# Kernel tuning notes

Measured on AMD Instinct MI355X. Metric: run time of the kernel, lower is better.

Reference implementation:

```python
import jax, jax.numpy as jnp
import numpy as np

ALPHA = 0.5    # SpikeAct surrogate width (act_fun(alpha=0.5))
DECAY = 0.2    # membrane decay
THRESH = 0.5   # firing threshold (requires_grad=False -> constant)


@jax.custom_vjp
def spike_act(x):
    # Heaviside spike with rectangular surrogate gradient
    return (x > 0).astype(x.dtype)

def _sa_fwd(x):
    return spike_act(x), x

def _sa_bwd(x, g):
    return (g * (jnp.abs(x) < ALPHA).astype(g.dtype),)

spike_act.defvjp(_sa_fwd, _sa_bwd)


@jax.custom_vjp
def ei_act(x):
    # EI sign gate with straight-through gradient
    return jnp.sign(x)

def _ei_fwd(x):
    return ei_act(x), None

def _ei_bwd(_, g):
    return (g,)

ei_act.defvjp(_ei_fwd, _ei_bwd)


def conv2d(x, w, b):
    # x: [B,C,H,W], w: [O,I,kh,kw] (OIHW), SAME padding, stride 1
    y = jax.lax.conv_general_dilated(
        x, w, window_strides=(1, 1), padding='SAME',
        dimension_numbers=('NCHW', 'OIHW', 'NCHW'))
    return y + b[None, :, None, None]


def setup_inputs() -> dict:
    key = jax.random.key(0)
    k0, k1, k2 = jax.random.split(key, 3)
    T, B, C, H, W, K = 8, 16, 128, 32, 32, 5
    fan_in = C * K * K
    x = jax.random.normal(k0, (T, B, C, H, W), jnp.float32)
    back_w = jax.random.normal(k1, (C, C, K, K), jnp.float32) / np.float32(np.sqrt(fan_in))
    back_b = jnp.zeros((C,), jnp.float32)
    ei_w = jax.random.normal(k2, (C, C, K, K), jnp.float32) / np.float32(np.sqrt(fan_in))
    ei_b = jnp.zeros((C,), jnp.float32)
    return {"x": x, "back_w": back_w, "back_b": back_b, "ei_w": ei_w, "ei_b": ei_b}


def reference(x, back_w, back_b, ei_w, ei_b):
    # x: [T,B,C,H,W] -> spikes over time [T,B,C,H,W]
    state_shape = x.shape[1:]
    mem0 = jnp.zeros(state_shape, x.dtype)
    spike0 = jnp.zeros(state_shape, x.dtype)

    def step(carry, xt):
        mem, spike = carry
        # integral: decayed mem + feedback-conv sigmoid gate * input
        mem = DECAY * mem + jax.nn.sigmoid(conv2d(spike, back_w, back_b)) * xt
        # calc_spike (if_ei=True path)
        ei_gate = ei_act(conv2d(mem, ei_w, ei_b))
        s = spike_act(mem - THRESH)
        mem = mem * (1.0 - s)
        spike = ei_gate * s
        return (mem, spike), spike

    _, spikes = jax.lax.scan(step, (mem0, spike0), x)
    return spikes
```

## Files before the change

### kernel.cpp

```cpp
#include <hip/hip_runtime.h>
#include <math.h>

#define TDIM 512
#define CCH  128
#define HW   32
#define OCT  4
#define NPH  32
#define PSW  36
#define PPL  1296
#define NCHK 11
#define LDSPH 2816


__device__ __forceinline__ void gll16(const float* g, float* l) {
    __builtin_amdgcn_global_load_lds(
        (const __attribute__((address_space(1))) unsigned int*)g,
        (__attribute__((address_space(3))) unsigned int*)l, 16, 0, 0);
}

template<int EPI>
__global__ __launch_bounds__(TDIM, 2) void lif_conv(
    const float* __restrict__ cpad,
    const float* __restrict__ wgt,
    const float* __restrict__ bias,
    const float* __restrict__ xin,
    float* __restrict__ pad0,
    float* __restrict__ outn,
    float* __restrict__ pad1,
    int first)
{
    const int ocg  = blockIdx.x;
    const int b    = blockIdx.y;
    const int oc0  = ocg * OCT;
    const int tid  = threadIdx.x;
    const int team = tid >> 8;
    const int lt   = tid & 255;
    const int rl   = lt >> 3;
    const int cl   = (lt & 7) * 4;
    const int wv   = (tid >> 6) & 3;
    const int lane = tid & 63;

    const int steam = __builtin_amdgcn_readfirstlane(team);

    __shared__ __align__(16) float s_in[2 * 2 * LDSPH];

    float acc[OCT][4];
#pragma unroll
    for (int oc = 0; oc < OCT; ++oc)
#pragma unroll
        for (int j = 0; j < 4; ++j) acc[oc][j] = 0.f;

    if (!(EPI == 0 && first)) {
        const int icb  = team * 64;
        const int sicb = steam * 64;
        float* lbase = s_in + steam * (2 * LDSPH);

        {
            const float* ps = cpad + ((size_t)b * CCH + icb) * PPL;
            for (int j = wv; j < NCHK; j += 4)
                gll16(ps + j * 256 + lane * 4, lbase + j * 256);
        }

        for (int ph = 0; ph < NPH; ++ph) {
            __syncthreads();
            if (ph < NPH - 1) {
                const float* ps = cpad + ((size_t)b * CCH + icb + (ph + 1) * 2) * PPL;
                float* ld = lbase + ((ph + 1) & 1) * LDSPH;
                for (int j = wv; j < NCHK; j += 4)
                    gll16(ps + j * 256 + lane * 4, ld + j * 256);
            }
            const float* tin = lbase + (ph & 1) * LDSPH;
#pragma unroll
            for (int ici = 0; ici < 2; ++ici) {
                float win5[5][8];
#pragma unroll
                for (int kh = 0; kh < 5; ++kh) {
                    const float* src = tin + ici * PPL + (rl + kh) * PSW + cl;
                    float4 a  = *(const float4*)src;
                    float4 c2 = *(const float4*)(src + 4);
                    win5[kh][0] = a.x;  win5[kh][1] = a.y;  win5[kh][2] = a.z;  win5[kh][3] = a.w;
                    win5[kh][4] = c2.x; win5[kh][5] = c2.y; win5[kh][6] = c2.z; win5[kh][7] = c2.w;
                }
                const float* wb = wgt + ((size_t)oc0 * CCH + sicb + ph * 2 + ici) * 25;
#pragma unroll
                for (int oc = 0; oc < OCT; ++oc) {
                    const float* wo = wb + oc * (CCH * 25);
#pragma unroll
                    for (int kh = 0; kh < 5; ++kh) {
#pragma unroll
                        for (int kw = 0; kw < 5; ++kw) {
                            float wv2 = wo[kh * 5 + kw];
                            acc[oc][0] += win5[kh][kw]     * wv2;
                            acc[oc][1] += win5[kh][kw + 1] * wv2;
                            acc[oc][2] += win5[kh][kw + 2] * wv2;
                            acc[oc][3] += win5[kh][kw + 3] * wv2;
                        }
                    }
                }
            }
        }

        __syncthreads();
        float* sred = s_in;
        if (team == 1) {
#pragma unroll
            for (int oc = 0; oc < OCT; ++oc)
#pragma unroll
                for (int j = 0; j < 4; ++j)
                    sred[lt * 17 + oc * 4 + j] = acc[oc][j];
        }
        __syncthreads();
        if (team == 0) {
#pragma unroll
            for (int oc = 0; oc < OCT; ++oc)
#pragma unroll
                for (int j = 0; j < 4; ++j)
                    acc[oc][j] += sred[lt * 17 + oc * 4 + j];
        }
    }

    if (team == 0) {
#pragma unroll
        for (int oc = 0; oc < OCT; ++oc) {
            const size_t pidxn = (((size_t)b * CCH + oc0 + oc) * HW + rl) * HW + cl;
            const size_t pidxp = ((size_t)b * CCH + oc0 + oc) * PPL + (rl + 2) * PSW + 2 + cl;
            const float bia = bias[oc0 + oc];
            float y[4];
#pragma unroll
            for (int j = 0; j < 4; ++j) y[j] = acc[oc][j] + bia;
            if (EPI == 0) {
                float4 xv = *(const float4*)(xin + pidxn);
                float xr[4] = {xv.x, xv.y, xv.z, xv.w};
                float mo[4] = {0.f, 0.f, 0.f, 0.f};
                if (!first) {
                    float2 a = *(const float2*)(pad0 + pidxp);
                    float2 c = *(const float2*)(pad0 + pidxp + 2);
                    mo[0] = a.x; mo[1] = a.y; mo[2] = c.x; mo[3] = c.y;
                }
                float mp[4];
#pragma unroll
                for (int j = 0; j < 4; ++j) {
                    float mv = (mo[j] > 0.5f) ? 0.f : mo[j];
                    mp[j] = 0.2f * mv + (1.f / (1.f + expf(-y[j]))) * xr[j];
                }
                *(float2*)(pad0 + pidxp)     = make_float2(mp[0], mp[1]);
                *(float2*)(pad0 + pidxp + 2) = make_float2(mp[2], mp[3]);
            } else {
                float2 a = *(const float2*)(pad0 + pidxp);
                float2 c = *(const float2*)(pad0 + pidxp + 2);
                float m[4] = {a.x, a.y, c.x, c.y};
                float sp[4];
#pragma unroll
                for (int j = 0; j < 4; ++j) {
                    float g = (y[j] > 0.f) ? 1.f : ((y[j] < 0.f) ? -1.f : 0.f);
                    float s = (m[j] > 0.5f) ? 1.f : 0.f;
                    sp[j] = g * s;
                }
                *(float4*)(outn + pidxn) = make_float4(sp[0], sp[1], sp[2], sp[3]);
                *(float2*)(pad1 + pidxp)     = make_float2(sp[0], sp[1]);
                *(float2*)(pad1 + pidxp + 2) = make_float2(sp[2], sp[3]);
            }
        }
    }
}

extern "C" void kernel_launch(void* const* d_in, const int* in_sizes, int n_in,
                              void* d_out, int out_size, void* d_ws, size_t ws_size,
                              hipStream_t stream) {
    const float* x      = (const float*)d_in[0];
    const float* back_w = (const float*)d_in[1];
    const float* back_b = (const float*)d_in[2];
    const float* ei_w   = (const float*)d_in[3];
    const float* ei_b   = (const float*)d_in[4];
    float* out = (float*)d_out;

    const size_t N     = (size_t)16 * CCH * HW * HW;
    const size_t PADSZ = (size_t)16 * CCH * PPL;
    float* pad0 = (float*)d_ws;
    float* pad1 = pad0 + PADSZ;

    hipMemsetAsync(d_ws, 0, 2 * PADSZ * sizeof(float), stream);

    dim3 grid(CCH / OCT, 16);

    for (int t = 0; t < 8; ++t) {
        lif_conv<0><<<grid, TDIM, 0, stream>>>(
            pad1, back_w, back_b,
            x + (size_t)t * N,
            pad0, nullptr, nullptr, (t == 0) ? 1 : 0);
        lif_conv<1><<<grid, TDIM, 0, stream>>>(
            pad0, ei_w, ei_b,
            nullptr,
            pad0, out + (size_t)t * N, pad1, 0);
    }
}
```

Measured before the change: 2.272 ms.

## Restructure conv blocks: 1024 threads, 8 output channels, per-wave slabs, split-K reduction

Each block now has 1024 threads and handles 8 output channels, which halves the grid. Each wave stages its own row-slab of one input channel into private LDS double buffers using waitcnt. This removes the block-wide __syncthreads on every phase. The input channels are split four ways across wave groups, and partial sums are combined with a tree reduction through LDS. Each block gets more weight reuse and less barrier overhead, at the cost of fewer blocks, higher register pressure, and extra halo loads for each slab.

```diff
diff --git a/kernel.cpp b/kernel.cpp
--- a/kernel.cpp
+++ b/kernel.cpp
@@ -1,16 +1,13 @@
 #include <hip/hip_runtime.h>
 #include <math.h>
 
-#define TDIM 512
 #define CCH  128
 #define HW   32
-#define OCT  4
+#define OCT  8
 #define NPH  32
 #define PSW  36
 #define PPL  1296
-#define NCHK 11
-#define LDSPH 2816
-
+#define SLAB 432
 
 __device__ __forceinline__ void gll16(const float* g, float* l) {
     __builtin_amdgcn_global_load_lds(
@@ -19,7 +16,7 @@
 }
 
 template<int EPI>
-__global__ __launch_bounds__(TDIM, 2) void lif_conv(
+__global__ __launch_bounds__(1024, 4) void lif_conv(
     const float* __restrict__ cpad,
     const float* __restrict__ wgt,
     const float* __restrict__ bias,
@@ -33,16 +30,18 @@
     const int b    = blockIdx.y;
     const int oc0  = ocg * OCT;
     const int tid  = threadIdx.x;
-    const int team = tid >> 8;
-    const int lt   = tid & 255;
-    const int rl   = lt >> 3;
-    const int cl   = (lt & 7) * 4;
-    const int wv   = (tid >> 6) & 3;
+    const int w    = tid >> 6;
     const int lane = tid & 63;
-
-    const int steam = __builtin_amdgcn_readfirstlane(team);
-
-    __shared__ __align__(16) float s_in[2 * 2 * LDSPH];
+    const int ks   = w >> 2;
+    const int rg   = w & 3;
+    const int rl   = lane >> 3;
+    const int cl   = (lane & 7) * 4;
+
+    const int sw  = __builtin_amdgcn_readfirstlane(w);
+    const int sks = sw >> 2;
+    const int srg = sw & 3;
+
+    __shared__ __align__(16) float s_in[16 * 2 * SLAB];
 
     float acc[OCT][4];
 #pragma unroll
@@ -51,79 +50,133 @@
         for (int j = 0; j < 4; ++j) acc[oc][j] = 0.f;
 
     if (!(EPI == 0 && first)) {
-        const int icb  = team * 64;
-        const int sicb = steam * 64;
-        float* lbase = s_in + steam * (2 * LDSPH);
-
-        {
-            const float* ps = cpad + ((size_t)b * CCH + icb) * PPL;
-            for (int j = wv; j < NCHK; j += 4)
-                gll16(ps + j * 256 + lane * 4, lbase + j * 256);
+        const float* pbase = cpad + ((size_t)b * CCH + sks * 32) * PPL + srg * 288;
+        float* bufA = s_in + sw * (2 * SLAB);
+        float* bufB = bufA + SLAB;
+
+        auto STAGE = [&](int ph, float* dst) {
+            const float* ps = pbase + (size_t)ph * PPL;
+            gll16(ps + lane * 4, dst);
+            if (lane < 44) gll16(ps + 256 + lane * 4, dst + 256);
+        };
+        auto COMPUTE = [&](int ph, const float* tin) {
+            float win[5][8];
+#pragma unroll
+            for (int kh = 0; kh < 5; ++kh) {
+                const float* src = tin + (rl + kh) * PSW + cl;
+                float4 a = *(const float4*)src;
+                float4 c = *(const float4*)(src + 4);
+                win[kh][0] = a.x; win[kh][1] = a.y; win[kh][2] = a.z; win[kh][3] = a.w;
+                win[kh][4] = c.x; win[kh][5] = c.y; win[kh][6] = c.z; win[kh][7] = c.w;
+            }
+            const float* wb = wgt + ((size_t)oc0 * CCH + sks * 32 + ph) * 25;
+#pragma unroll
+            for (int oc = 0; oc < OCT; ++oc) {
+                const float* wo = wb + oc * (CCH * 25);
+#pragma unroll
+                for (int kh = 0; kh < 5; ++kh) {
+#pragma unroll
+                    for (int kw = 0; kw < 5; ++kw) {
+                        float wv = wo[kh * 5 + kw];
+                        acc[oc][0] += win[kh][kw]     * wv;
+                        acc[oc][1] += win[kh][kw + 1] * wv;
+                        acc[oc][2] += win[kh][kw + 2] * wv;
+                        acc[oc][3] += win[kh][kw + 3] * wv;
+                    }
+                }
+            }
+        };
+
+        STAGE(0, bufA);
+        for (int ph = 0; ph < NPH; ph += 2) {
+            STAGE(ph + 1, bufB);
+            asm volatile("s_waitcnt vmcnt(2)" ::: "memory");
+            __builtin_amdgcn_sched_barrier(0);
+            COMPUTE(ph, bufA);
+            if (ph + 2 < NPH) {
+                STAGE(ph + 2, bufA);
+                asm volatile("s_waitcnt vmcnt(2)" ::: "memory");
+            } else {
+                asm volatile("s_waitcnt vmcnt(0)" ::: "memory");
+            }
+            __builtin_amdgcn_sched_barrier(0);
+            COMPUTE(ph + 1, bufB);
         }
 
-        for (int ph = 0; ph < NPH; ++ph) {
-            __syncthreads();
-            if (ph < NPH - 1) {
-                const float* ps = cpad + ((size_t)b * CCH + icb + (ph + 1) * 2) * PPL;
-                float* ld = lbase + ((ph + 1) & 1) * LDSPH;
-                for (int j = wv; j < NCHK; j += 4)
-                    gll16(ps + j * 256 + lane * 4, ld + j * 256);
-            }
-            const float* tin = lbase + (ph & 1) * LDSPH;
-#pragma unroll
-            for (int ici = 0; ici < 2; ++ici) {
-                float win5[5][8];
-#pragma unroll
-                for (int kh = 0; kh < 5; ++kh) {
-                    const float* src = tin + ici * PPL + (rl + kh) * PSW + cl;
-                    float4 a  = *(const float4*)src;
-                    float4 c2 = *(const float4*)(src + 4);
-                    win5[kh][0] = a.x;  win5[kh][1] = a.y;  win5[kh][2] = a.z;  win5[kh][3] = a.w;
-                    win5[kh][4] = c2.x; win5[kh][5] = c2.y; win5[kh][6] = c2.z; win5[kh][7] = c2.w;
-                }
-                const float* wb = wgt + ((size_t)oc0 * CCH + sicb + ph * 2 + ici) * 25;
-#pragma unroll
-                for (int oc = 0; oc < OCT; ++oc) {
-                    const float* wo = wb + oc * (CCH * 25);
-#pragma unroll
-                    for (int kh = 0; kh < 5; ++kh) {
-#pragma unroll
-                        for (int kw = 0; kw < 5; ++kw) {
-                            float wv2 = wo[kh * 5 + kw];
-                            acc[oc][0] += win5[kh][kw]     * wv2;
-                            acc[oc][1] += win5[kh][kw + 1] * wv2;
-                            acc[oc][2] += win5[kh][kw + 2] * wv2;
-                            acc[oc][3] += win5[kh][kw + 3] * wv2;
-                        }
-                    }
-                }
-            }
+        __syncthreads();
+        const int key = (rg * 64 + lane) * 17;
+        float* A = s_in;
+        float* B = s_in + 4352;
+        if (ks == 3)
+#pragma unroll
+            for (int oc = 0; oc < 4; ++oc)
+#pragma unroll
+                for (int j = 0; j < 4; ++j) A[key + oc * 4 + j] = acc[oc][j];
+        if (ks == 2)
+#pragma unroll
+            for (int oc = 0; oc < 4; ++oc)
+#pragma unroll
+                for (int j = 0; j < 4; ++j) B[key + oc * 4 + j] = acc[oc][j];
+        __syncthreads();
+        if (ks == 1)
+#pragma unroll
+            for (int oc = 0; oc < 4; ++oc)
+#pragma unroll
+                for (int j = 0; j < 4; ++j) acc[oc][j] += A[key + oc * 4 + j];
+        if (ks == 0)
+#pragma unroll
+            for (int oc = 0; oc < 4; ++oc)
+#pragma unroll
+                for (int j = 0; j < 4; ++j) acc[oc][j] += B[key + oc * 4 + j];
+        __syncthreads();
+        if (ks == 3)
+#pragma unroll
+            for (int oc = 4; oc < 8; ++oc)
+#pragma unroll
+                for (int j = 0; j < 4; ++j) A[key + (oc - 4) * 4 + j] = acc[oc][j];
+        if (ks == 2)
+#pragma unroll
+            for (int oc = 4; oc < 8; ++oc)
+#pragma unroll
+                for (int j = 0; j < 4; ++j) B[key + (oc - 4) * 4 + j] = acc[oc][j];
+        __syncthreads();
+        if (ks == 1)
+#pragma unroll
+            for (int oc = 4; oc < 8; ++oc)
+#pragma unroll
+                for (int j = 0; j < 4; ++j) acc[oc][j] += A[key + (oc - 4) * 4 + j];
+        if (ks == 0)
+#pragma unroll
+            for (int oc = 4; oc < 8; ++oc)
+#pragma unroll
+                for (int j = 0; j < 4; ++j) acc[oc][j] += B[key + (oc - 4) * 4 + j];
+        __syncthreads();
+        if (ks == 1) {
+#pragma unroll
+            for (int oc = 0; oc < 4; ++oc)
+#pragma unroll
+                for (int j = 0; j < 4; ++j) {
+                    A[key + oc * 4 + j] = acc[oc][j];
+                    B[key + oc * 4 + j] = acc[oc + 4][j];
+                }
         }
-
-        __syncthreads();
-        float* sred = s_in;
-        if (team == 1) {
-#pragma unroll
-            for (int oc = 0; oc < OCT; ++oc)
-#pragma unroll
-                for (int j = 0; j < 4; ++j)
-                    sred[lt * 17 + oc * 4 + j] = acc[oc][j];
-        }
-        __syncthreads();
-        if (team == 0) {
-#pragma unroll
-            for (int oc = 0; oc < OCT; ++oc)
-#pragma unroll
-                for (int j = 0; j < 4; ++j)
-                    acc[oc][j] += sred[lt * 17 + oc * 4 + j];
-        }
+        __syncthreads();
+        if (ks == 0)
+#pragma unroll
+            for (int oc = 0; oc < 4; ++oc)
+#pragma unroll
+                for (int j = 0; j < 4; ++j) {
+                    acc[oc][j]     += A[key + oc * 4 + j];
+                    acc[oc + 4][j] += B[key + oc * 4 + j];
+                }
     }
 
-    if (team == 0) {
+    if (ks == 0) {
+        const int row = rg * 8 + rl;
 #pragma unroll
         for (int oc = 0; oc < OCT; ++oc) {
-            const size_t pidxn = (((size_t)b * CCH + oc0 + oc) * HW + rl) * HW + cl;
-            const size_t pidxp = ((size_t)b * CCH + oc0 + oc) * PPL + (rl + 2) * PSW + 2 + cl;
+            const size_t pidxn = (((size_t)b * CCH + oc0 + oc) * HW + row) * HW + cl;
+            const size_t pidxp = ((size_t)b * CCH + oc0 + oc) * PPL + (row + 2) * PSW + 2 + cl;
             const float bia = bias[oc0 + oc];
             float y[4];
 #pragma unroll
@@ -182,13 +235,12 @@
     hipMemsetAsync(d_ws, 0, 2 * PADSZ * sizeof(float), stream);
 
     dim3 grid(CCH / OCT, 16);
-
     for (int t = 0; t < 8; ++t) {
-        lif_conv<0><<<grid, TDIM, 0, stream>>>(
+        lif_conv<0><<<grid, 1024, 0, stream>>>(
             pad1, back_w, back_b,
             x + (size_t)t * N,
             pad0, nullptr, nullptr, (t == 0) ? 1 : 0);
-        lif_conv<1><<<grid, TDIM, 0, stream>>>(
+        lif_conv<1><<<grid, 1024, 0, stream>>>(
             pad0, ei_w, ei_b,
             nullptr,
             pad0, out + (size_t)t * N, pad1, 0);
```

Result: slower. 2.863 ms (+26.0%).
